# Kernel optimization log

Hardware: AMD Instinct MI355X
Metric: run time of the kernel (lower is better)

Reference implementation:

```python
import jax, jax.numpy as jnp
import numpy as np

N, E, F = 50000, 400000, 32

_WN = ["w10","w11","w20","w21","w30","w31","w40","w41","wl01","wl02","wl1","wl2"]
_BN = ["b10","b11","b20","b21","b30","b31","b40","b41","bl01","bl02","bl1","bl2"]
_DIMS = [(4,F),(F,F),(2*F+F+4,F),(F,F),(6*F,F),(F,F),(6*F,F),(F,F),(F,F),(F,F),(F,4),(F,1)]


def _lin(key, fin, fout):
    kw, kb = jax.random.split(key)
    w = jax.random.normal(kw, (fin, fout), jnp.float32) / np.float32(np.sqrt(fin))
    b = jax.random.normal(kb, (fout,), jnp.float32) * 0.01
    return w, b


def setup_inputs() -> dict:
    key = jax.random.key(0)
    ks = jax.random.split(key, 5)
    inp = {}
    inp["x"] = jax.random.normal(ks[0], (N, 4), jnp.float32)
    inp["edge_index"] = jax.random.randint(ks[1], (2, E), 0, N, jnp.int32)
    inp["edge_attr"] = jax.random.normal(ks[2], (E, 4), jnp.float32)
    inp["beta"] = jax.random.normal(ks[3], (N, 3), jnp.float32)
    lkeys = jax.random.split(ks[4], len(_DIMS))
    for i, (fin, fout) in enumerate(_DIMS):
        w, b = _lin(lkeys[i], fin, fout)
        inp[_WN[i]] = w
        inp[_BN[i]] = b
    return inp


def reference(x, edge_index, edge_attr, beta,
              w10, b10, w11, b11, w20, b20, w21, b21,
              w30, b30, w31, b31, w40, b40, w41, b41,
              wl01, bl01, wl02, bl02, wl1, bl1, wl2, bl2):
    row, col = edge_index[0], edge_index[1]
    n = x.shape[0]

    def mlp2(m, w0, b0, w1, b1):
        return jax.nn.relu(m @ w0 + b0) @ w1 + b1

    def seg_mean(h):  # scatter-mean onto target nodes (row), dim_size=n
        s = jax.ops.segment_sum(h, row, num_segments=n)
        c = jax.ops.segment_sum(jnp.ones((h.shape[0], 1), h.dtype), row, num_segments=n)
        return s / jnp.maximum(c, 1.0)

    # conv1: x is zeros with dim 4 (<=5), so message = mlp0(edge_attr)
    e1 = mlp2(edge_attr, w10, b10, w11, b11)            # [E,32]
    x1 = jax.nn.relu(seg_mean(e1)); e1 = jax.nn.relu(e1)
    # conv2
    ea2 = jnp.concatenate([edge_attr, e1], axis=1)      # [E,36]
    e2 = mlp2(jnp.concatenate([x1[row], x1[col], ea2], axis=1), w20, b20, w21, b21)
    x2 = jax.nn.relu(seg_mean(e2)); e2 = jax.nn.relu(e2)
    # conv3
    x21 = jnp.concatenate([x2, x1], axis=1)             # [N,64]
    ea3 = jnp.concatenate([e2, e1], axis=1)             # [E,64]
    e3 = mlp2(jnp.concatenate([x21[row], x21[col], ea3], axis=1), w30, b30, w31, b31)
    x3 = jax.nn.relu(seg_mean(e3)); e3 = jax.nn.relu(e3)
    # conv4 (node aggregate x4 is never used downstream, so skipped)
    x32 = jnp.concatenate([x3, x2], axis=1)
    ea4 = jnp.concatenate([e3, e2], axis=1)
    e4 = jax.nn.relu(mlp2(jnp.concatenate([x32[row], x32[col], ea4], axis=1), w40, b40, w41, b41))
    # heads
    out01 = e4 @ wl01 + bl01
    out02 = e4 @ wl02 + bl02
    edge_x = out01 @ wl1 + bl1 + edge_attr
    edge_x = edge_x / jnp.maximum(jnp.linalg.norm(edge_x, axis=1, keepdims=True), 1e-12)
    probs = jax.nn.sigmoid(out02 @ wl2 + bl2)           # [E,1]
    return (probs, edge_x, beta)
```

## Files before the change

### kernel.cpp

```cpp
#include <hip/hip_runtime.h>
#include <hip/hip_bf16.h>

#define EE 400000
#define NN 50000
#define NCH 8
#define CHUNK (EE / NCH)
#define NTOT (NCH * NN)
#define SCAN_NBLK ((NTOT + 1023) / 1024)
#define NTILES (EE / 16)
#define TPX (NTILES / 8)
#define NPTILES ((NN + 15) / 16)

typedef float f32x4 __attribute__((ext_vector_type(4)));
typedef __bf16 bf16x8 __attribute__((ext_vector_type(8)));
typedef unsigned int u32;
typedef unsigned int u32x4 __attribute__((ext_vector_type(4)));

static __device__ __forceinline__ bf16x8 u4_as_bf8(u32x4 u) {
  return __builtin_bit_cast(bf16x8, u);
}
static __device__ __forceinline__ u32 relu_pk2(u32 d) {
  u32 m = (d & 0x80008000u) >> 15;
  m ^= 0x00010001u;
  return d & ((m << 16) - m);
}
static __device__ __forceinline__ u32 pk2bf(float a, float b) {
  union { __bf16 h[2]; u32 w; } t;
  t.h[0] = (__bf16)a; t.h[1] = (__bf16)b;
  return t.w;
}

__global__ void init_kernel(int* __restrict__ count,
                            const float* __restrict__ bl01, const float* __restrict__ bl02,
                            const float* __restrict__ wl1,  const float* __restrict__ bl1,
                            const float* __restrict__ wl2,  const float* __restrict__ bl2,
                            float* __restrict__ headw) {
  int i = blockIdx.x * blockDim.x + threadIdx.x;
  if (i < NTOT) count[i] = 0;
  if (blockIdx.x == 0) {
    int t = threadIdx.x;
    if (t < 4) {
      float s = bl1[t];
      for (int j = 0; j < 32; ++j) s += bl01[j] * wl1[j * 4 + t];
      headw[160 + t] = s;
    } else if (t == 4) {
      float s = bl2[0];
      for (int j = 0; j < 32; ++j) s += bl02[j] * wl2[j];
      headw[164] = s;
    }
  }
}

__global__ void pack_all_kernel(const float* __restrict__ w10, const float* __restrict__ w11,
                                const float* __restrict__ w20, const float* __restrict__ w21,
                                const float* __restrict__ w30, const float* __restrict__ w31,
                                const float* __restrict__ w40, const float* __restrict__ w41,
                                const float* __restrict__ wl01, const float* __restrict__ wl1,
                                const float* __restrict__ wl02, const float* __restrict__ wl2,
                                __bf16* __restrict__ pk) {
  const int f = blockIdx.x;
  const int t = threadIdx.x;
  int stage, lf;
  const float *W0, *W1;
  if (f < 4)       { stage = 1; lf = f;      W0 = w10; W1 = w11; }
  else if (f < 14) { stage = 2; lf = f - 4;  W0 = w20; W1 = w21; }
  else if (f < 28) { stage = 3; lf = f - 14; W0 = w30; W1 = w31; }
  else             { stage = 4; lf = f - 28; W0 = w40; W1 = w41; }
#pragma unroll
  for (int u = 0; u < 2; ++u) {
    int idx = t * 2 + u;
    int lane = idx >> 3, i = idx & 7;
    int l15 = lane & 15, g = lane >> 4;
    int k = 8 * g + i;
    float v = 0.f;
    if (stage == 1) {
      if (lf < 2)      v = (k < 4) ? W0[k * 32 + lf * 16 + l15] : 0.f;
      else             v = W1[k * 32 + (lf - 2) * 16 + l15];
    } else if (stage == 2) {
      if (lf < 4)      { int part = lf >> 1, nb = lf & 1; v = W0[(part * 32 + k) * 32 + nb * 16 + l15]; }
      else if (lf < 6) { int nb = lf - 4; v = (k < 4) ? W0[(64 + k) * 32 + nb * 16 + l15] : 0.f; }
      else if (lf < 8) { int nb = lf - 6; v = W0[(68 + k) * 32 + nb * 16 + l15]; }
      else             { int nb = lf - 8; v = W1[k * 32 + nb * 16 + l15]; }
    } else {
      if (lf < 8)       { int part = lf >> 2, kb = (lf >> 1) & 1, nb = lf & 1;
                          v = W0[(part * 64 + kb * 32 + k) * 32 + nb * 16 + l15]; }
      else if (lf < 12) { int eb = (lf - 8) >> 1, nb = lf & 1;
                          v = W0[(128 + eb * 32 + k) * 32 + nb * 16 + l15]; }
      else if (lf < 14) { int nb = lf - 12; v = W1[k * 32 + nb * 16 + l15]; }
      else {
        if (l15 < 4)      { float s = 0.f; for (int j = 0; j < 32; ++j) s += wl01[k * 32 + j] * wl1[j * 4 + l15]; v = s; }
        else if (l15 == 4){ float s = 0.f; for (int j = 0; j < 32; ++j) s += wl02[k * 32 + j] * wl2[j]; v = s; }
      }
    }
    pk[f * 512 + idx] = (__bf16)v;
  }
}

__global__ void hist_kernel(const int* __restrict__ rowi, int* __restrict__ count) {
  const int c = blockIdx.x & 7;
  const int lb = blockIdx.x >> 3;
  const int nb = gridDim.x >> 3;
  for (int i = lb * blockDim.x + threadIdx.x; i < CHUNK; i += nb * blockDim.x) {
    int e = c * CHUNK + i;
    atomicAdd(&count[c * NN + rowi[e]], 1);
  }
}

__global__ void scanA_kernel(const int* __restrict__ count, int* __restrict__ offs,
                             int* __restrict__ partial) {
  __shared__ int lds[1024];
  const int t = threadIdx.x;
  const int i = blockIdx.x * 1024 + t;
  int v = (i < NTOT) ? count[i] : 0;
  lds[t] = v;
  __syncthreads();
  for (int off = 1; off < 1024; off <<= 1) {
    int u = (t >= off) ? lds[t - off] : 0;
    __syncthreads();
    lds[t] += u;
    __syncthreads();
  }
  int incl = lds[t];
  if (i < NTOT) offs[i] = incl - v;
  if (t == 1023) partial[blockIdx.x] = incl;
}

__global__ void scanB_kernel(const int* __restrict__ partial, int* __restrict__ offs,
                             int* __restrict__ cursor) {
  __shared__ int sbase;
  const int t = threadIdx.x;
  const int b = blockIdx.x;
  if (t < 64) {
    int s = 0;
    for (int j = t; j < b; j += 64) s += partial[j];
#pragma unroll
    for (int o = 32; o > 0; o >>= 1) s += __shfl_down(s, o);
    if (t == 0) sbase = s;
  }
  __syncthreads();
  const int base = sbase;
  const int i = b * 1024 + t;
  if (i < NTOT) {
    int o = offs[i] + base;
    offs[i] = o;
    cursor[i] = o;
  }
  if (b == 0 && t == 0) offs[NTOT] = EE;
}

__global__ void scatter_kernel(const int* __restrict__ rowi, const int* __restrict__ coli,
                               const float* __restrict__ eattr, int* __restrict__ cursor,
                               uint4* __restrict__ record, int* __restrict__ inv) {
  const int c = blockIdx.x & 7;
  const int lb = blockIdx.x >> 3;
  const int nb = gridDim.x >> 3;
  for (int i = lb * blockDim.x + threadIdx.x; i < CHUNK; i += nb * blockDim.x) {
    int e = c * CHUNK + i;
    int r = rowi[e];
    int p = atomicAdd(&cursor[c * NN + r], 1);
    inv[e] = p;
    const float4 v = *(const float4*)(eattr + (size_t)e * 4);
    uint4 rec;
    rec.x = (u32)r;
    rec.y = (u32)coli[e];
    rec.z = pk2bf(v.x, v.y);
    rec.w = pk2bf(v.z, v.w);
    record[p] = rec;
  }
}

__global__ void agg_kernel(const __bf16* __restrict__ esrc,
                           const int* __restrict__ offs,
                           __bf16* __restrict__ dst1, int s1, int o1,
                           __bf16* __restrict__ dst2, int s2, int o2) {
  int idx = blockIdx.x * blockDim.x + threadIdx.x;
  int n = idx >> 6;
  int half = (idx >> 5) & 1;
  int j = idx & 31;
  if (n >= NN) return;
  float s = 0.f;
  int cnt = 0;
#pragma unroll
  for (int cc = 0; cc < 4; ++cc) {
    int c = half * 4 + cc;
    int a = offs[c * NN + n], b = offs[c * NN + n + 1];
    cnt += b - a;
    for (int t = a; t < b; ++t)
      s += (float)esrc[(size_t)t * 32 + j];
  }
  s += __shfl_xor(s, 32);
  cnt += __shfl_xor(cnt, 32);
  float mean = s / fmaxf((float)cnt, 1.f);
  __bf16 x = (__bf16)fmaxf(mean, 0.f);
  if (half == 0) dst1[(size_t)n * s1 + o1 + j] = x;
  else if (dst2) dst2[(size_t)n * s2 + o2 + j] = x;
}

template <int NPK>
__launch_bounds__(256, 4)
__global__ void nodeproj_kernel(const __bf16* __restrict__ pk,
                                const __bf16* __restrict__ xcat, int xoff, int xstride,
                                __bf16* __restrict__ ur, __bf16* __restrict__ uc) {
  constexpr int NKB = NPK / 32;
  const int tid = threadIdx.x;
  const int lane = tid & 63;
  const int wid = tid >> 6;
  const int l15 = lane & 15;
  const int g = lane >> 4;

  bf16x8 Br[NKB][2], Bc[NKB][2];
#pragma unroll
  for (int kb = 0; kb < NKB; ++kb)
#pragma unroll
    for (int nb = 0; nb < 2; ++nb) {
      Br[kb][nb] = *(const bf16x8*)(pk + (size_t)((0 * NKB + kb) * 2 + nb) * 512 + lane * 8);
      Bc[kb][nb] = *(const bf16x8*)(pk + (size_t)((1 * NKB + kb) * 2 + nb) * 512 + lane * 8);
    }

  const int t = blockIdx.x * 4 + wid;
  if (t >= NPTILES) return;
  const int base = t * 16;
  const int n = base + l15;
  const int nc = (n < NN) ? n : (NN - 1);

  f32x4 r0 = {0,0,0,0}, r1 = {0,0,0,0}, c0 = {0,0,0,0}, c1 = {0,0,0,0};
#pragma unroll
  for (int kb = 0; kb < NKB; ++kb) {
    bf16x8 a = *(const bf16x8*)(xcat + (size_t)nc * xstride + xoff + kb * 32 + 8 * g);
    r0 = __builtin_amdgcn_mfma_f32_16x16x32_bf16(a, Br[kb][0], r0, 0, 0, 0);
    r1 = __builtin_amdgcn_mfma_f32_16x16x32_bf16(a, Br[kb][1], r1, 0, 0, 0);
    c0 = __builtin_amdgcn_mfma_f32_16x16x32_bf16(a, Bc[kb][0], c0, 0, 0, 0);
    c1 = __builtin_amdgcn_mfma_f32_16x16x32_bf16(a, Bc[kb][1], c1, 0, 0, 0);
  }
#pragma unroll
  for (int r = 0; r < 4; ++r) {
    int m = 4 * g + r;
    if (base + m < NN) {
      size_t row = (size_t)(base + m) * 32;
      ur[row + l15]      = (__bf16)r0[r];
      ur[row + 16 + l15] = (__bf16)r1[r];
      uc[row + l15]      = (__bf16)c0[r];
      uc[row + 16 + l15] = (__bf16)c1[r];
    }
  }
}

template <int STAGE>
__launch_bounds__(256, 5)
__global__ void conv_kernel(const __bf16* __restrict__ pk,
                            const float* __restrict__ B0, const float* __restrict__ B1v,
                            const uint4* __restrict__ record,
                            const __bf16* __restrict__ ur,
                            const __bf16* __restrict__ uc,
                            const __bf16* __restrict__ ein1,
                            const __bf16* __restrict__ ein2,
                            __bf16* __restrict__ d1,
                            const float* __restrict__ headw,
                            float* __restrict__ tmpP, float* __restrict__ tmpEX) {
  constexpr int NEB  = (STAGE == 1) ? 1 : 2;
  constexpr int FEB  = (STAGE == 1) ? 0 : (STAGE == 2) ? 4 : 8;
  constexpr int FW1  = (STAGE == 1) ? 2 : (STAGE == 2) ? 8 : 12;
  __shared__ __align__(16) float ldsH[4 * 16 * 36];

  const int tid = threadIdx.x;
  const int lane = tid & 63;
  const int wid = tid >> 6;
  const int l15 = lane & 15;
  const int g = lane >> 4;

  bf16x8 Bf[NEB][2];
#pragma unroll
  for (int eb = 0; eb < NEB; ++eb)
#pragma unroll
    for (int nb = 0; nb < 2; ++nb)
      Bf[eb][nb] = *(const bf16x8*)(pk + (size_t)(FEB + eb * 2 + nb) * 512 + lane * 8);
  bf16x8 B2f[2];
#pragma unroll
  for (int nb = 0; nb < 2; ++nb)
    B2f[nb] = *(const bf16x8*)(pk + (size_t)(FW1 + nb) * 512 + lane * 8);

  bf16x8 I0, I1;
#pragma unroll
  for (int i = 0; i < 8; ++i) {
    int k = 8 * g + i;
    I0[i] = (k == l15)      ? (__bf16)1.0f : (__bf16)0.0f;
    I1[i] = (k == 16 + l15) ? (__bf16)1.0f : (__bf16)0.0f;
  }

  const float b0j0 = B0[l15], b0j1 = B0[l15 + 16];
  const float b1j0 = B1v[l15], b1j1 = B1v[l15 + 16];

  bf16x8 Bh;
  float bexc = 0.f, bp = 0.f;
  if (STAGE == 4) {
    Bh = *(const bf16x8*)(pk + (size_t)14 * 512 + lane * 8);
    if (l15 < 4) bexc = headw[160 + l15];
    bp = headw[164];
  }

  float* hl = &ldsH[wid * 576];

  const int xcd = blockIdx.x & 7;
  const int wloc = (blockIdx.x >> 3) * 4 + wid;
  const int nwl = (gridDim.x >> 3) * 4;
  for (int t0 = wloc; t0 < TPX; t0 += nwl) {
    const int t = xcd * TPX + t0;
    const int base = t * 16;
    const int p = base + l15;

    const uint4 rec = record[p];

    bf16x8 urf, ucf;
    if (STAGE >= 2) {
      int rid = (int)rec.x, cid = (int)rec.y;
      urf = *(const bf16x8*)(ur + (size_t)rid * 32 + 8 * g);
      ucf = *(const bf16x8*)(uc + (size_t)cid * 32 + 8 * g);
    }

    bf16x8 ae;
    if (STAGE <= 2) {
      u32x4 u = {0, 0, 0, 0};
      if (g == 0) { u.x = rec.z; u.y = rec.w; }
      ae = u4_as_bf8(u);
    }

    f32x4 a0a = {0,0,0,0}, a0b = {0,0,0,0}, a1a = {0,0,0,0}, a1b = {0,0,0,0};
    if (STAGE >= 2) {
      a0a = __builtin_amdgcn_mfma_f32_16x16x32_bf16(urf, I0, a0a, 0, 0, 0);
      a1a = __builtin_amdgcn_mfma_f32_16x16x32_bf16(urf, I1, a1a, 0, 0, 0);
      a0a = __builtin_amdgcn_mfma_f32_16x16x32_bf16(ucf, I0, a0a, 0, 0, 0);
      a1a = __builtin_amdgcn_mfma_f32_16x16x32_bf16(ucf, I1, a1a, 0, 0, 0);
    }
#pragma unroll
    for (int eb = 0; eb < NEB; ++eb) {
      bf16x8 a;
      if (STAGE == 1) {
        a = ae;
      } else if (STAGE == 2) {
        if (eb == 0) a = ae;
        else {
          u32x4 u = *(const u32x4*)(ein1 + (size_t)p * 32 + 8 * g);
          u.x = relu_pk2(u.x); u.y = relu_pk2(u.y); u.z = relu_pk2(u.z); u.w = relu_pk2(u.w);
          a = u4_as_bf8(u);
        }
      } else {
        const __bf16* src = (eb == 0) ? ein1 : ein2;
        u32x4 u = *(const u32x4*)(src + (size_t)p * 32 + 8 * g);
        u.x = relu_pk2(u.x); u.y = relu_pk2(u.y); u.z = relu_pk2(u.z); u.w = relu_pk2(u.w);
        a = u4_as_bf8(u);
      }
      a0b = __builtin_amdgcn_mfma_f32_16x16x32_bf16(a, Bf[eb][0], a0b, 0, 0, 0);
      a1b = __builtin_amdgcn_mfma_f32_16x16x32_bf16(a, Bf[eb][1], a1b, 0, 0, 0);
    }
    f32x4 acc0 = a0a + a0b, acc1 = a1a + a1b;

#pragma unroll
    for (int r = 0; r < 4; ++r) {
      int m = 4 * g + r;
      hl[m * 36 + l15]      = fmaxf(acc0[r] + b0j0, 0.f);
      hl[m * 36 + l15 + 16] = fmaxf(acc1[r] + b0j1, 0.f);
    }
    f32x4 h0 = *(const f32x4*)&hl[l15 * 36 + 8 * g];
    f32x4 h1 = *(const f32x4*)&hl[l15 * 36 + 8 * g + 4];
    bf16x8 a2;
#pragma unroll
    for (int i = 0; i < 4; ++i) { a2[i] = (__bf16)h0[i]; a2[i + 4] = (__bf16)h1[i]; }
    f32x4 o0 = {0,0,0,0}, o1 = {0,0,0,0};
    o0 = __builtin_amdgcn_mfma_f32_16x16x32_bf16(a2, B2f[0], o0, 0, 0, 0);
    o1 = __builtin_amdgcn_mfma_f32_16x16x32_bf16(a2, B2f[1], o1, 0, 0, 0);

    if (STAGE <= 3) {
#pragma unroll
      for (int r = 0; r < 4; ++r) {
        int m = 4 * g + r;
        size_t eo = (size_t)(base + m) * 32;
        d1[eo + l15]      = (__bf16)(o0[r] + b1j0);
        d1[eo + l15 + 16] = (__bf16)(o1[r] + b1j1);
      }
    } else {
#pragma unroll
      for (int r = 0; r < 4; ++r) {
        int m = 4 * g + r;
        hl[m * 36 + l15]      = fmaxf(o0[r] + b1j0, 0.f);
        hl[m * 36 + l15 + 16] = fmaxf(o1[r] + b1j1, 0.f);
      }
      f32x4 q0 = *(const f32x4*)&hl[l15 * 36 + 8 * g];
      f32x4 q1 = *(const f32x4*)&hl[l15 * 36 + 8 * g + 4];
      bf16x8 a3;
#pragma unroll
      for (int i = 0; i < 4; ++i) { a3[i] = (__bf16)q0[i]; a3[i + 4] = (__bf16)q1[i]; }
      f32x4 ho = {0,0,0,0};
      ho = __builtin_amdgcn_mfma_f32_16x16x32_bf16(a3, Bh, ho, 0, 0, 0);
#pragma unroll
      for (int r = 0; r < 4; ++r) {
        int m = 4 * g + r;
        int po = base + m;
        float s = ho[r];
        u32 zz = __shfl(rec.z, m);
        u32 ww = __shfl(rec.w, m);
        float v = 0.f, sq = 0.f;
        if (l15 < 4) {
          u32 wzw = (l15 & 2) ? ww : zz;
          u32 bits = (l15 & 1) ? (wzw & 0xffff0000u) : (wzw << 16);
          v = s + bexc + __uint_as_float(bits);
          sq = v * v;
        }
        sq += __shfl_xor(sq, 1);
        sq += __shfl_xor(sq, 2);
        if (l15 < 4) tmpEX[(size_t)po * 4 + l15] = v * (1.f / fmaxf(sqrtf(sq), 1e-12f));
        if (l15 == 4) tmpP[po] = 1.f / (1.f + __expf(-(s + bp)));
      }
    }
  }
}

__global__ void unpermute_kernel(const int* __restrict__ inv,
                                 const float* __restrict__ tmpP,
                                 const float* __restrict__ tmpEX,
                                 const float* __restrict__ beta,
                                 float* __restrict__ outP, float* __restrict__ outEX,
                                 float* __restrict__ outB) {
  int e = blockIdx.x * blockDim.x + threadIdx.x;
  if (e >= EE) return;
  int p = inv[e];
  outP[e] = tmpP[p];
  float4 ex = *(const float4*)(tmpEX + (size_t)p * 4);
  *(float4*)(outEX + (size_t)e * 4) = ex;
  if (e < NN * 3) outB[e] = beta[e];
}

extern "C" void kernel_launch(void* const* d_in, const int* in_sizes, int n_in,
                              void* d_out, int out_size, void* d_ws, size_t ws_size,
                              hipStream_t stream) {
  const float* eattr = (const float*)d_in[2];
  const float* beta = (const float*)d_in[3];
  const float* w10 = (const float*)d_in[4];  const float* b10 = (const float*)d_in[5];
  const float* w11 = (const float*)d_in[6];  const float* b11 = (const float*)d_in[7];
  const float* w20 = (const float*)d_in[8];  const float* b20 = (const float*)d_in[9];
  const float* w21 = (const float*)d_in[10]; const float* b21 = (const float*)d_in[11];
  const float* w30 = (const float*)d_in[12]; const float* b30 = (const float*)d_in[13];
  const float* w31 = (const float*)d_in[14]; const float* b31 = (const float*)d_in[15];
  const float* w40 = (const float*)d_in[16]; const float* b40 = (const float*)d_in[17];
  const float* w41 = (const float*)d_in[18]; const float* b41 = (const float*)d_in[19];
  const float* wl01 = (const float*)d_in[20]; const float* bl01 = (const float*)d_in[21];
  const float* wl02 = (const float*)d_in[22]; const float* bl02 = (const float*)d_in[23];
  const float* wl1 = (const float*)d_in[24];  const float* bl1 = (const float*)d_in[25];
  const float* wl2 = (const float*)d_in[26];  const float* bl2 = (const float*)d_in[27];
  const int* rowi = (const int*)d_in[1];
  const int* coli = rowi + EE;

  char* w = (char*)d_ws;
  auto alloc = [&](size_t bytes) {
    char* p = w;
    w += (bytes + 255) & ~(size_t)255;
    return p;
  };
  __bf16* e1b = (__bf16*)alloc((size_t)EE * 32 * 2);
  __bf16* e2b = (__bf16*)alloc((size_t)EE * 32 * 2);
  __bf16* e3b = (__bf16*)alloc((size_t)EE * 32 * 2);
  __bf16* ur  = (__bf16*)alloc((size_t)NN * 32 * 2);
  __bf16* uc  = (__bf16*)alloc((size_t)NN * 32 * 2);
  __bf16* x21 = (__bf16*)alloc((size_t)NN * 64 * 2);
  __bf16* x32 = (__bf16*)alloc((size_t)NN * 64 * 2);
  int* count = (int*)alloc(NTOT * 4);
  int* offs = (int*)alloc((NTOT + 1) * 4);
  int* cursor = (int*)alloc(NTOT * 4);
  int* inv = (int*)alloc(EE * 4);
  uint4* record = (uint4*)alloc((size_t)EE * 16);
  float* tmpP = (float*)alloc((size_t)EE * 4);
  float* tmpEX = (float*)alloc((size_t)EE * 4 * 4);
  float* headw = (float*)alloc(256 * 4);
  int* partial = (int*)alloc(512 * 4);
  __bf16* packw = (__bf16*)alloc((size_t)43 * 512 * 2);

  float* outP = (float*)d_out;
  float* outEX = outP + EE;
  float* outB = outP + (size_t)5 * EE;

  __bf16* pk1 = packw;
  __bf16* pk2 = packw + 4 * 512;
  __bf16* pk3 = packw + 14 * 512;
  __bf16* pk4 = packw + 28 * 512;

  init_kernel<<<(NTOT + 255) / 256, 256, 0, stream>>>(count, bl01, bl02, wl1, bl1, wl2, bl2, headw);
  pack_all_kernel<<<43, 256, 0, stream>>>(w10, w11, w20, w21, w30, w31, w40, w41,
                                          wl01, wl1, wl02, wl2, packw);
  hist_kernel<<<1024, 256, 0, stream>>>(rowi, count);
  scanA_kernel<<<SCAN_NBLK, 1024, 0, stream>>>(count, offs, partial);
  scanB_kernel<<<SCAN_NBLK, 1024, 0, stream>>>(partial, offs, cursor);
  scatter_kernel<<<1024, 256, 0, stream>>>(rowi, coli, eattr, cursor, record, inv);

  conv_kernel<1><<<2048, 256, 0, stream>>>(pk1, b10, b11, record,
                                           (const __bf16*)nullptr, (const __bf16*)nullptr,
                                           (const __bf16*)nullptr, (const __bf16*)nullptr, e1b,
                                           (const float*)nullptr, (float*)nullptr, (float*)nullptr);
  agg_kernel<<<(NN * 64 + 255) / 256, 256, 0, stream>>>(e1b, offs, x21, 64, 32,
                                                        (__bf16*)nullptr, 0, 0);
  nodeproj_kernel<32><<<(NPTILES + 3) / 4, 256, 0, stream>>>(pk2, x21, 32, 64, ur, uc);
  conv_kernel<2><<<2048, 256, 0, stream>>>(pk2, b20, b21, record,
                                           ur, uc, e1b, (const __bf16*)nullptr, e2b,
                                           (const float*)nullptr, (float*)nullptr, (float*)nullptr);
  agg_kernel<<<(NN * 64 + 255) / 256, 256, 0, stream>>>(e2b, offs, x21, 64, 0, x32, 64, 32);
  nodeproj_kernel<64><<<(NPTILES + 3) / 4, 256, 0, stream>>>(pk3, x21, 0, 64, ur, uc);
  conv_kernel<3><<<2048, 256, 0, stream>>>(pk3, b30, b31, record,
                                           ur, uc, e2b, e1b, e3b,
                                           (const float*)nullptr, (float*)nullptr, (float*)nullptr);
  agg_kernel<<<(NN * 64 + 255) / 256, 256, 0, stream>>>(e3b, offs, x32, 64, 0,
                                                        (__bf16*)nullptr, 0, 0);
  nodeproj_kernel<64><<<(NPTILES + 3) / 4, 256, 0, stream>>>(pk4, x32, 0, 64, ur, uc);
  conv_kernel<4><<<2048, 256, 0, stream>>>(pk4, b40, b41, record,
                                           ur, uc, e3b, e2b, (__bf16*)nullptr,
                                           headw, tmpP, tmpEX);
  unpermute_kernel<<<(EE + 255) / 256, 256, 0, stream>>>(inv, tmpP, tmpEX, beta,
                                                         outP, outEX, outB);
}
```

Measured before the change: 239.1 us.

## Merge init and pack kernels, prefetch edge records, shrink conv grid

Fuses the count-zeroing/head-bias init kernel with the weight packing kernel to save one launch. In the conv kernels, the next tile's edge record is software-prefetched one iteration ahead so the dependent gather of node projections is not serialized behind the record load. The conv grid shrinks from 2048 to 1280 blocks, so each wave handles more tiles and amortizes per-wave setup, with a risk of lower latency hiding. The prefetch costs extra registers.

```diff
diff --git a/kernel.cpp b/kernel.cpp
--- a/kernel.cpp
+++ b/kernel.cpp
@@ -10,6 +10,7 @@
 #define NTILES (EE / 16)
 #define TPX (NTILES / 8)
 #define NPTILES ((NN + 15) / 16)
+#define INIT_NBLK ((NTOT + 255) / 256)
 
 typedef float f32x4 __attribute__((ext_vector_type(4)));
 typedef __bf16 bf16x8 __attribute__((ext_vector_type(8)));
@@ -30,36 +31,34 @@
   return t.w;
 }
 
-__global__ void init_kernel(int* __restrict__ count,
-                            const float* __restrict__ bl01, const float* __restrict__ bl02,
-                            const float* __restrict__ wl1,  const float* __restrict__ bl1,
-                            const float* __restrict__ wl2,  const float* __restrict__ bl2,
-                            float* __restrict__ headw) {
-  int i = blockIdx.x * blockDim.x + threadIdx.x;
-  if (i < NTOT) count[i] = 0;
-  if (blockIdx.x == 0) {
-    int t = threadIdx.x;
-    if (t < 4) {
-      float s = bl1[t];
-      for (int j = 0; j < 32; ++j) s += bl01[j] * wl1[j * 4 + t];
-      headw[160 + t] = s;
-    } else if (t == 4) {
-      float s = bl2[0];
-      for (int j = 0; j < 32; ++j) s += bl02[j] * wl2[j];
-      headw[164] = s;
-    }
-  }
-}
-
-__global__ void pack_all_kernel(const float* __restrict__ w10, const float* __restrict__ w11,
-                                const float* __restrict__ w20, const float* __restrict__ w21,
-                                const float* __restrict__ w30, const float* __restrict__ w31,
-                                const float* __restrict__ w40, const float* __restrict__ w41,
-                                const float* __restrict__ wl01, const float* __restrict__ wl1,
-                                const float* __restrict__ wl02, const float* __restrict__ wl2,
-                                __bf16* __restrict__ pk) {
+__global__ void init_pack_kernel(const float* __restrict__ w10, const float* __restrict__ w11,
+                                 const float* __restrict__ w20, const float* __restrict__ w21,
+                                 const float* __restrict__ w30, const float* __restrict__ w31,
+                                 const float* __restrict__ w40, const float* __restrict__ w41,
+                                 const float* __restrict__ wl01, const float* __restrict__ wl1,
+                                 const float* __restrict__ wl02, const float* __restrict__ wl2,
+                                 const float* __restrict__ bl01, const float* __restrict__ bl02,
+                                 const float* __restrict__ bl1, const float* __restrict__ bl2,
+                                 __bf16* __restrict__ pk,
+                                 int* __restrict__ count, float* __restrict__ headw) {
+  const int t = threadIdx.x;
+  if (blockIdx.x >= 43) {
+    int i = (blockIdx.x - 43) * 256 + t;
+    if (i < NTOT) count[i] = 0;
+    if (blockIdx.x == 43) {
+      if (t < 4) {
+        float s = bl1[t];
+        for (int j = 0; j < 32; ++j) s += bl01[j] * wl1[j * 4 + t];
+        headw[160 + t] = s;
+      } else if (t == 4) {
+        float s = bl2[0];
+        for (int j = 0; j < 32; ++j) s += bl02[j] * wl2[j];
+        headw[164] = s;
+      }
+    }
+    return;
+  }
   const int f = blockIdx.x;
-  const int t = threadIdx.x;
   int stage, lf;
   const float *W0, *W1;
   if (f < 4)       { stage = 1; lf = f;      W0 = w10; W1 = w11; }
@@ -301,18 +300,24 @@
   float* hl = &ldsH[wid * 576];
 
   const int xcd = blockIdx.x & 7;
-  const int wloc = (blockIdx.x >> 3) * 4 + wid;
   const int nwl = (gridDim.x >> 3) * 4;
-  for (int t0 = wloc; t0 < TPX; t0 += nwl) {
+  int t0 = (blockIdx.x >> 3) * 4 + wid;
+
+  uint4 rec;
+  if (t0 < TPX) rec = record[(size_t)(xcd * TPX + t0) * 16 + l15];
+
+  for (; t0 < TPX; t0 += nwl) {
     const int t = xcd * TPX + t0;
     const int base = t * 16;
     const int p = base + l15;
 
-    const uint4 rec = record[p];
+    const uint4 recc = rec;
+    { int t1 = t0 + nwl;
+      if (t1 < TPX) rec = record[(size_t)(xcd * TPX + t1) * 16 + l15]; }
 
     bf16x8 urf, ucf;
     if (STAGE >= 2) {
-      int rid = (int)rec.x, cid = (int)rec.y;
+      int rid = (int)recc.x, cid = (int)recc.y;
       urf = *(const bf16x8*)(ur + (size_t)rid * 32 + 8 * g);
       ucf = *(const bf16x8*)(uc + (size_t)cid * 32 + 8 * g);
     }
@@ -320,7 +325,7 @@
     bf16x8 ae;
     if (STAGE <= 2) {
       u32x4 u = {0, 0, 0, 0};
-      if (g == 0) { u.x = rec.z; u.y = rec.w; }
+      if (g == 0) { u.x = recc.z; u.y = recc.w; }
       ae = u4_as_bf8(u);
     }
 
@@ -396,8 +401,8 @@
         int m = 4 * g + r;
         int po = base + m;
         float s = ho[r];
-        u32 zz = __shfl(rec.z, m);
-        u32 ww = __shfl(rec.w, m);
+        u32 zz = __shfl(recc.z, m);
+        u32 ww = __shfl(recc.w, m);
         float v = 0.f, sq = 0.f;
         if (l15 < 4) {
           u32 wzw = (l15 & 2) ? ww : zz;
@@ -482,33 +487,33 @@
   __bf16* pk3 = packw + 14 * 512;
   __bf16* pk4 = packw + 28 * 512;
 
-  init_kernel<<<(NTOT + 255) / 256, 256, 0, stream>>>(count, bl01, bl02, wl1, bl1, wl2, bl2, headw);
-  pack_all_kernel<<<43, 256, 0, stream>>>(w10, w11, w20, w21, w30, w31, w40, w41,
-                                          wl01, wl1, wl02, wl2, packw);
+  init_pack_kernel<<<43 + INIT_NBLK, 256, 0, stream>>>(
+      w10, w11, w20, w21, w30, w31, w40, w41, wl01, wl1, wl02, wl2,
+      bl01, bl02, bl1, bl2, packw, count, headw);
   hist_kernel<<<1024, 256, 0, stream>>>(rowi, count);
   scanA_kernel<<<SCAN_NBLK, 1024, 0, stream>>>(count, offs, partial);
   scanB_kernel<<<SCAN_NBLK, 1024, 0, stream>>>(partial, offs, cursor);
   scatter_kernel<<<1024, 256, 0, stream>>>(rowi, coli, eattr, cursor, record, inv);
 
-  conv_kernel<1><<<2048, 256, 0, stream>>>(pk1, b10, b11, record,
+  conv_kernel<1><<<1280, 256, 0, stream>>>(pk1, b10, b11, record,
                                            (const __bf16*)nullptr, (const __bf16*)nullptr,
                                            (const __bf16*)nullptr, (const __bf16*)nullptr, e1b,
                                            (const float*)nullptr, (float*)nullptr, (float*)nullptr);
   agg_kernel<<<(NN * 64 + 255) / 256, 256, 0, stream>>>(e1b, offs, x21, 64, 32,
                                                         (__bf16*)nullptr, 0, 0);
   nodeproj_kernel<32><<<(NPTILES + 3) / 4, 256, 0, stream>>>(pk2, x21, 32, 64, ur, uc);
-  conv_kernel<2><<<2048, 256, 0, stream>>>(pk2, b20, b21, record,
+  conv_kernel<2><<<1280, 256, 0, stream>>>(pk2, b20, b21, record,
                                            ur, uc, e1b, (const __bf16*)nullptr, e2b,
                                            (const float*)nullptr, (float*)nullptr, (float*)nullptr);
   agg_kernel<<<(NN * 64 + 255) / 256, 256, 0, stream>>>(e2b, offs, x21, 64, 0, x32, 64, 32);
   nodeproj_kernel<64><<<(NPTILES + 3) / 4, 256, 0, stream>>>(pk3, x21, 0, 64, ur, uc);
-  conv_kernel<3><<<2048, 256, 0, stream>>>(pk3, b30, b31, record,
+  conv_kernel<3><<<1280, 256, 0, stream>>>(pk3, b30, b31, record,
                                            ur, uc, e2b, e1b, e3b,
                                            (const float*)nullptr, (float*)nullptr, (float*)nullptr);
   agg_kernel<<<(NN * 64 + 255) / 256, 256, 0, stream>>>(e3b, offs, x32, 64, 0,
                                                         (__bf16*)nullptr, 0, 0);
   nodeproj_kernel<64><<<(NPTILES + 3) / 4, 256, 0, stream>>>(pk4, x32, 0, 64, ur, uc);
-  conv_kernel<4><<<2048, 256, 0, stream>>>(pk4, b40, b41, record,
+  conv_kernel<4><<<1280, 256, 0, stream>>>(pk4, b40, b41, record,
                                            ur, uc, e3b, e2b, (__bf16*)nullptr,
                                            headw, tmpP, tmpEX);
   unpermute_kernel<<<(EE + 255) / 256, 256, 0, stream>>>(inv, tmpP, tmpEX, beta,
```

Result: slower. 245.8 us (+2.8%).

## Replace 8-chunk CSR sort with single global row-sorted CSR and merge init kernels

Applied to the files above, without the earlier changes.

Drops the per-chunk (8-way) counting sort in favour of a single node-indexed histogram, scan and scatter, so each node's edges form one contiguous segment. The aggregation kernel then reads a single offset range per node with 32 threads instead of 64 threads over four chunk ranges plus a shuffle reduction. The init and weight-pack kernels are merged into one launch, and hist/scatter use one thread per edge. The cost is more atomic contention per counter, and the per-node edge order inside a segment becomes nondeterministic, which can change which edges sit adjacent in the conv tiles.

```diff
diff --git a/kernel.cpp b/kernel.cpp
--- a/kernel.cpp
+++ b/kernel.cpp
@@ -3,13 +3,11 @@
 
 #define EE 400000
 #define NN 50000
-#define NCH 8
-#define CHUNK (EE / NCH)
-#define NTOT (NCH * NN)
-#define SCAN_NBLK ((NTOT + 1023) / 1024)
+#define SCAN_NBLK ((NN + 1023) / 1024)
 #define NTILES (EE / 16)
 #define TPX (NTILES / 8)
 #define NPTILES ((NN + 15) / 16)
+#define INIT_NBLK ((NN + 255) / 256)
 
 typedef float f32x4 __attribute__((ext_vector_type(4)));
 typedef __bf16 bf16x8 __attribute__((ext_vector_type(8)));
@@ -30,36 +28,34 @@
   return t.w;
 }
 
-__global__ void init_kernel(int* __restrict__ count,
-                            const float* __restrict__ bl01, const float* __restrict__ bl02,
-                            const float* __restrict__ wl1,  const float* __restrict__ bl1,
-                            const float* __restrict__ wl2,  const float* __restrict__ bl2,
-                            float* __restrict__ headw) {
-  int i = blockIdx.x * blockDim.x + threadIdx.x;
-  if (i < NTOT) count[i] = 0;
-  if (blockIdx.x == 0) {
-    int t = threadIdx.x;
-    if (t < 4) {
-      float s = bl1[t];
-      for (int j = 0; j < 32; ++j) s += bl01[j] * wl1[j * 4 + t];
-      headw[160 + t] = s;
-    } else if (t == 4) {
-      float s = bl2[0];
-      for (int j = 0; j < 32; ++j) s += bl02[j] * wl2[j];
-      headw[164] = s;
-    }
-  }
-}
-
-__global__ void pack_all_kernel(const float* __restrict__ w10, const float* __restrict__ w11,
-                                const float* __restrict__ w20, const float* __restrict__ w21,
-                                const float* __restrict__ w30, const float* __restrict__ w31,
-                                const float* __restrict__ w40, const float* __restrict__ w41,
-                                const float* __restrict__ wl01, const float* __restrict__ wl1,
-                                const float* __restrict__ wl02, const float* __restrict__ wl2,
-                                __bf16* __restrict__ pk) {
+__global__ void init_pack_kernel(const float* __restrict__ w10, const float* __restrict__ w11,
+                                 const float* __restrict__ w20, const float* __restrict__ w21,
+                                 const float* __restrict__ w30, const float* __restrict__ w31,
+                                 const float* __restrict__ w40, const float* __restrict__ w41,
+                                 const float* __restrict__ wl01, const float* __restrict__ wl1,
+                                 const float* __restrict__ wl02, const float* __restrict__ wl2,
+                                 const float* __restrict__ bl01, const float* __restrict__ bl02,
+                                 const float* __restrict__ bl1, const float* __restrict__ bl2,
+                                 __bf16* __restrict__ pk,
+                                 int* __restrict__ count, float* __restrict__ headw) {
+  const int t = threadIdx.x;
+  if (blockIdx.x >= 43) {
+    int i = (blockIdx.x - 43) * 256 + t;
+    if (i < NN) count[i] = 0;
+    if (blockIdx.x == 43) {
+      if (t < 4) {
+        float s = bl1[t];
+        for (int j = 0; j < 32; ++j) s += bl01[j] * wl1[j * 4 + t];
+        headw[160 + t] = s;
+      } else if (t == 4) {
+        float s = bl2[0];
+        for (int j = 0; j < 32; ++j) s += bl02[j] * wl2[j];
+        headw[164] = s;
+      }
+    }
+    return;
+  }
   const int f = blockIdx.x;
-  const int t = threadIdx.x;
   int stage, lf;
   const float *W0, *W1;
   if (f < 4)       { stage = 1; lf = f;      W0 = w10; W1 = w11; }
@@ -97,13 +93,8 @@
 }
 
 __global__ void hist_kernel(const int* __restrict__ rowi, int* __restrict__ count) {
-  const int c = blockIdx.x & 7;
-  const int lb = blockIdx.x >> 3;
-  const int nb = gridDim.x >> 3;
-  for (int i = lb * blockDim.x + threadIdx.x; i < CHUNK; i += nb * blockDim.x) {
-    int e = c * CHUNK + i;
-    atomicAdd(&count[c * NN + rowi[e]], 1);
-  }
+  int e = blockIdx.x * blockDim.x + threadIdx.x;
+  if (e < EE) atomicAdd(&count[rowi[e]], 1);
 }
 
 __global__ void scanA_kernel(const int* __restrict__ count, int* __restrict__ offs,
@@ -111,7 +102,7 @@
   __shared__ int lds[1024];
   const int t = threadIdx.x;
   const int i = blockIdx.x * 1024 + t;
-  int v = (i < NTOT) ? count[i] : 0;
+  int v = (i < NN) ? count[i] : 0;
   lds[t] = v;
   __syncthreads();
   for (int off = 1; off < 1024; off <<= 1) {
@@ -121,7 +112,7 @@
     __syncthreads();
   }
   int incl = lds[t];
-  if (i < NTOT) offs[i] = incl - v;
+  if (i < NN) offs[i] = incl - v;
   if (t == 1023) partial[blockIdx.x] = incl;
 }
 
@@ -140,33 +131,29 @@
   __syncthreads();
   const int base = sbase;
   const int i = b * 1024 + t;
-  if (i < NTOT) {
+  if (i < NN) {
     int o = offs[i] + base;
     offs[i] = o;
     cursor[i] = o;
   }
-  if (b == 0 && t == 0) offs[NTOT] = EE;
+  if (b == 0 && t == 0) offs[NN] = EE;
 }
 
 __global__ void scatter_kernel(const int* __restrict__ rowi, const int* __restrict__ coli,
                                const float* __restrict__ eattr, int* __restrict__ cursor,
                                uint4* __restrict__ record, int* __restrict__ inv) {
-  const int c = blockIdx.x & 7;
-  const int lb = blockIdx.x >> 3;
-  const int nb = gridDim.x >> 3;
-  for (int i = lb * blockDim.x + threadIdx.x; i < CHUNK; i += nb * blockDim.x) {
-    int e = c * CHUNK + i;
-    int r = rowi[e];
-    int p = atomicAdd(&cursor[c * NN + r], 1);
-    inv[e] = p;
-    const float4 v = *(const float4*)(eattr + (size_t)e * 4);
-    uint4 rec;
-    rec.x = (u32)r;
-    rec.y = (u32)coli[e];
-    rec.z = pk2bf(v.x, v.y);
-    rec.w = pk2bf(v.z, v.w);
-    record[p] = rec;
-  }
+  int e = blockIdx.x * blockDim.x + threadIdx.x;
+  if (e >= EE) return;
+  int r = rowi[e];
+  int p = atomicAdd(&cursor[r], 1);
+  inv[e] = p;
+  const float4 v = *(const float4*)(eattr + (size_t)e * 4);
+  uint4 rec;
+  rec.x = (u32)r;
+  rec.y = (u32)coli[e];
+  rec.z = pk2bf(v.x, v.y);
+  rec.w = pk2bf(v.z, v.w);
+  record[p] = rec;
 }
 
 __global__ void agg_kernel(const __bf16* __restrict__ esrc,
@@ -174,26 +161,17 @@
                            __bf16* __restrict__ dst1, int s1, int o1,
                            __bf16* __restrict__ dst2, int s2, int o2) {
   int idx = blockIdx.x * blockDim.x + threadIdx.x;
-  int n = idx >> 6;
-  int half = (idx >> 5) & 1;
+  int n = idx >> 5;
   int j = idx & 31;
   if (n >= NN) return;
+  int a = offs[n], b = offs[n + 1];
   float s = 0.f;
-  int cnt = 0;
-#pragma unroll
-  for (int cc = 0; cc < 4; ++cc) {
-    int c = half * 4 + cc;
-    int a = offs[c * NN + n], b = offs[c * NN + n + 1];
-    cnt += b - a;
-    for (int t = a; t < b; ++t)
-      s += (float)esrc[(size_t)t * 32 + j];
-  }
-  s += __shfl_xor(s, 32);
-  cnt += __shfl_xor(cnt, 32);
-  float mean = s / fmaxf((float)cnt, 1.f);
+  for (int t = a; t < b; ++t)
+    s += (float)esrc[(size_t)t * 32 + j];
+  float mean = s / fmaxf((float)(b - a), 1.f);
   __bf16 x = (__bf16)fmaxf(mean, 0.f);
-  if (half == 0) dst1[(size_t)n * s1 + o1 + j] = x;
-  else if (dst2) dst2[(size_t)n * s2 + o2 + j] = x;
+  dst1[(size_t)n * s1 + o1 + j] = x;
+  if (dst2) dst2[(size_t)n * s2 + o2 + j] = x;
 }
 
 template <int NPK>
@@ -462,9 +440,9 @@
   __bf16* uc  = (__bf16*)alloc((size_t)NN * 32 * 2);
   __bf16* x21 = (__bf16*)alloc((size_t)NN * 64 * 2);
   __bf16* x32 = (__bf16*)alloc((size_t)NN * 64 * 2);
-  int* count = (int*)alloc(NTOT * 4);
-  int* offs = (int*)alloc((NTOT + 1) * 4);
-  int* cursor = (int*)alloc(NTOT * 4);
+  int* count = (int*)alloc(NN * 4);
+  int* offs = (int*)alloc((NN + 1) * 4);
+  int* cursor = (int*)alloc(NN * 4);
   int* inv = (int*)alloc(EE * 4);
   uint4* record = (uint4*)alloc((size_t)EE * 16);
   float* tmpP = (float*)alloc((size_t)EE * 4);
@@ -482,30 +460,31 @@
   __bf16* pk3 = packw + 14 * 512;
   __bf16* pk4 = packw + 28 * 512;
 
-  init_kernel<<<(NTOT + 255) / 256, 256, 0, stream>>>(count, bl01, bl02, wl1, bl1, wl2, bl2, headw);
-  pack_all_kernel<<<43, 256, 0, stream>>>(w10, w11, w20, w21, w30, w31, w40, w41,
-                                          wl01, wl1, wl02, wl2, packw);
-  hist_kernel<<<1024, 256, 0, stream>>>(rowi, count);
+  init_pack_kernel<<<43 + INIT_NBLK, 256, 0, stream>>>(
+      w10, w11, w20, w21, w30, w31, w40, w41, wl01, wl1, wl02, wl2,
+      bl01, bl02, bl1, bl2, packw, count, headw);
+  hist_kernel<<<(EE + 255) / 256, 256, 0, stream>>>(rowi, count);
   scanA_kernel<<<SCAN_NBLK, 1024, 0, stream>>>(count, offs, partial);
   scanB_kernel<<<SCAN_NBLK, 1024, 0, stream>>>(partial, offs, cursor);
-  scatter_kernel<<<1024, 256, 0, stream>>>(rowi, coli, eattr, cursor, record, inv);
+  scatter_kernel<<<(EE + 255) / 256, 256, 0, stream>>>(rowi, coli, eattr, cursor,
+                                                       record, inv);
 
   conv_kernel<1><<<2048, 256, 0, stream>>>(pk1, b10, b11, record,
                                            (const __bf16*)nullptr, (const __bf16*)nullptr,
                                            (const __bf16*)nullptr, (const __bf16*)nullptr, e1b,
                                            (const float*)nullptr, (float*)nullptr, (float*)nullptr);
-  agg_kernel<<<(NN * 64 + 255) / 256, 256, 0, stream>>>(e1b, offs, x21, 64, 32,
+  agg_kernel<<<(NN * 32 + 255) / 256, 256, 0, stream>>>(e1b, offs, x21, 64, 32,
                                                         (__bf16*)nullptr, 0, 0);
   nodeproj_kernel<32><<<(NPTILES + 3) / 4, 256, 0, stream>>>(pk2, x21, 32, 64, ur, uc);
   conv_kernel<2><<<2048, 256, 0, stream>>>(pk2, b20, b21, record,
                                            ur, uc, e1b, (const __bf16*)nullptr, e2b,
                                            (const float*)nullptr, (float*)nullptr, (float*)nullptr);
-  agg_kernel<<<(NN * 64 + 255) / 256, 256, 0, stream>>>(e2b, offs, x21, 64, 0, x32, 64, 32);
+  agg_kernel<<<(NN * 32 + 255) / 256, 256, 0, stream>>>(e2b, offs, x21, 64, 0, x32, 64, 32);
   nodeproj_kernel<64><<<(NPTILES + 3) / 4, 256, 0, stream>>>(pk3, x21, 0, 64, ur, uc);
   conv_kernel<3><<<2048, 256, 0, stream>>>(pk3, b30, b31, record,
                                            ur, uc, e2b, e1b, e3b,
                                            (const float*)nullptr, (float*)nullptr, (float*)nullptr);
-  agg_kernel<<<(NN * 64 + 255) / 256, 256, 0, stream>>>(e3b, offs, x32, 64, 0,
+  agg_kernel<<<(NN * 32 + 255) / 256, 256, 0, stream>>>(e3b, offs, x32, 64, 0,
                                                         (__bf16*)nullptr, 0, 0);
   nodeproj_kernel<64><<<(NPTILES + 3) / 4, 256, 0, stream>>>(pk4, x32, 0, 64, ur, uc);
   conv_kernel<4><<<2048, 256, 0, stream>>>(pk4, b40, b41, record,
```

Result: faster. 200.6 us (-16.1%).
